# Performance work log

Hardware: AMD Instinct MI355X
Metric: run time of the kernel (lower is better)

The kernel has to match this reference:

```python
import jax, jax.numpy as jnp
import numpy as np
import math

D_MODEL = 512
NUM_HEADS = 8
HEAD_DIM = D_MODEL // NUM_HEADS
B, L = 2, 2048
LN_EPS = 1e-5
DEN_EPS = 1e-5


def setup_inputs() -> dict:
    key = jax.random.key(0)
    ks = jax.random.split(key, 6)
    s = 1.0 / math.sqrt(D_MODEL)
    return {
        "x": jax.random.normal(ks[0], (B, L, D_MODEL), dtype=jnp.float32),
        "Wqkv": jax.random.normal(ks[1], (D_MODEL, 3 * D_MODEL), dtype=jnp.float32) * s,
        "bqkv": jnp.zeros((3 * D_MODEL,), dtype=jnp.float32),
        "Wout": jax.random.normal(ks[2], (D_MODEL, D_MODEL), dtype=jnp.float32) * s,
        "bout": jnp.zeros((D_MODEL,), dtype=jnp.float32),
        "ln_gamma": jnp.ones((D_MODEL,), dtype=jnp.float32),
        "ln_beta": jnp.zeros((D_MODEL,), dtype=jnp.float32),
        "decay_logits": jnp.full((NUM_HEADS,), 5.0, dtype=jnp.float32),
    }


def reference(x, Wqkv, bqkv, Wout, bout, ln_gamma, ln_beta, decay_logits):
    Bv, Lv, D = x.shape
    H = decay_logits.shape[0]
    E = D // H

    qkv = x @ Wqkv + bqkv                                   # [B,L,3D]
    q, k, v = jnp.split(qkv, 3, axis=-1)
    q = q.reshape(Bv, Lv, H, E)
    k = k.reshape(Bv, Lv, H, E)
    v = v.reshape(Bv, Lv, H, E)

    # ELU feature map + 1 -> positive features; scale q by 1/sqrt(E)
    q = (jax.nn.elu(q) + 1.0) / jnp.sqrt(jnp.asarray(E, x.dtype))
    k = jax.nn.elu(k) + 1.0

    lambdas = jax.nn.sigmoid(decay_logits).reshape(1, 1, H, 1)   # [1,1,H,1]
    t = jnp.arange(Lv, dtype=x.dtype).reshape(1, Lv, 1, 1)       # [1,L,1,1]
    decay_k = jnp.power(lambdas, -t)   # lambda^{-t}
    decay_q = jnp.power(lambdas, t)    # lambda^{t}

    k_dec = k * decay_k                                          # [B,L,H,E]
    kv = jnp.einsum('blhe,blhf->blhef', k_dec, v)                # [B,L,H,E,E]
    memory = jnp.cumsum(kv, axis=1)                              # prefix-sum scan over L
    k_sum = jnp.cumsum(k_dec, axis=1)                            # [B,L,H,E]

    q_dec = q * decay_q
    num = jnp.einsum('blhe,blhef->blhf', q_dec, memory)          # [B,L,H,E]
    den = jnp.einsum('blhe,blhe->blh', q_dec, k_sum)[..., None] + DEN_EPS
    out = (num / den).reshape(Bv, Lv, D)

    out = out @ Wout + bout

    # LayerNorm (eval mode; dropout is identity)
    mu = jnp.mean(out, axis=-1, keepdims=True)
    var = jnp.var(out, axis=-1, keepdims=True)
    out = (out - mu) / jnp.sqrt(var + LN_EPS) * ln_gamma + ln_beta
    return out
```

## Files before the change

### kernel.cpp

```cpp
#include <hip/hip_runtime.h>
#include <math.h>

#define B_ 2
#define L_ 2048
#define D_ 512
#define H_ 8
#define E_ 64
#define CHUNK 32
#define NCH 64
#define DEN_EPS_ 1e-5f
#define LN_EPS_ 1e-5f

typedef __bf16 bf16x8 __attribute__((ext_vector_type(8)));
typedef __bf16 bf16x4 __attribute__((ext_vector_type(4)));
typedef float  f32x4  __attribute__((ext_vector_type(4)));

__device__ __forceinline__ float sigm(float x) { return 1.f / (1.f + expf(-x)); }
__device__ __forceinline__ float elu1(float x) { return x > 0.f ? x + 1.f : expf(x); }

__global__ __launch_bounds__(256) void k_transpose_both(
    const float* __restrict__ W1, __bf16* __restrict__ D1,
    const float* __restrict__ W2, __bf16* __restrict__ D2)
{
    const float* src; __bf16* dst; int N;
    if (blockIdx.z == 0) { src = W1; dst = D1; N = 1536; }
    else                 { if (blockIdx.x >= 8) return; src = W2; dst = D2; N = 512; }
    const int K = 512;

    __shared__ __bf16 tile[64][68];
    const int kb = blockIdx.y * 64, nb = blockIdx.x * 64;
    const int t = threadIdx.x;
    const int rr = t >> 4, cc4 = (t & 15) * 4;
#pragma unroll
    for (int p = 0; p < 4; p++) {
        int k = rr + p * 16;
        float4 v = *(const float4*)&src[(size_t)(kb + k) * N + nb + cc4];
        tile[k][cc4 + 0] = (__bf16)v.x;
        tile[k][cc4 + 1] = (__bf16)v.y;
        tile[k][cc4 + 2] = (__bf16)v.z;
        tile[k][cc4 + 3] = (__bf16)v.w;
    }
    __syncthreads();
#pragma unroll
    for (int p = 0; p < 4; p++) {
        int n = rr + p * 16;
        bf16x4 o;
        o[0] = tile[cc4 + 0][n];
        o[1] = tile[cc4 + 1][n];
        o[2] = tile[cc4 + 2][n];
        o[3] = tile[cc4 + 3][n];
        *(bf16x4*)&dst[(size_t)(nb + n) * K + kb + cc4] = o;
    }
}

__global__ __launch_bounds__(256) void k_mfma_qkv(
    const float* __restrict__ X, const __bf16* __restrict__ Bt,
    const float* __restrict__ bias,
    __bf16* __restrict__ Qb, __bf16* __restrict__ Kb, __bf16* __restrict__ Vb)
{
    __shared__ __bf16 Al[128 * 32];
    __shared__ __bf16 Bl[128 * 32];
    const int t = threadIdx.x;
    const int w = t >> 6, lane = t & 63;
    const int wm = w >> 1, wn = w & 1;
    const int ll = lane & 15, quad = lane >> 4;
    const int m0 = blockIdx.y * 128, n0 = blockIdx.x * 128;

    f32x4 acc[4][4] = {};
    const int sr = t >> 2, sk = (t & 3) * 8;

    for (int k0 = 0; k0 < D_; k0 += 32) {
#pragma unroll
        for (int half = 0; half < 2; half++) {
            const float* ap = X + (size_t)(m0 + sr + half * 64) * D_ + k0 + sk;
            float4 a0 = *(const float4*)ap;
            float4 a1 = *(const float4*)(ap + 4);
            bf16x8 o;
            o[0] = (__bf16)a0.x; o[1] = (__bf16)a0.y; o[2] = (__bf16)a0.z; o[3] = (__bf16)a0.w;
            o[4] = (__bf16)a1.x; o[5] = (__bf16)a1.y; o[6] = (__bf16)a1.z; o[7] = (__bf16)a1.w;
            *(bf16x8*)&Al[(sr + half * 64) * 32 + sk] = o;
        }
        *(bf16x8*)&Bl[sr * 32 + sk]        = *(const bf16x8*)&Bt[(size_t)(n0 + sr) * D_ + k0 + sk];
        *(bf16x8*)&Bl[(sr + 64) * 32 + sk] = *(const bf16x8*)&Bt[(size_t)(n0 + sr + 64) * D_ + k0 + sk];
        __syncthreads();
#pragma unroll
        for (int im = 0; im < 4; im++) {
            bf16x8 a = *(const bf16x8*)&Al[(wm * 64 + im * 16 + ll) * 32 + quad * 8];
#pragma unroll
            for (int in = 0; in < 4; in++) {
                bf16x8 b = *(const bf16x8*)&Bl[(wn * 64 + in * 16 + ll) * 32 + quad * 8];
                acc[im][in] = __builtin_amdgcn_mfma_f32_16x16x32_bf16(a, b, acc[im][in], 0, 0, 0);
            }
        }
        __syncthreads();
    }

    const int sec = n0 >> 9;
    __bf16* base = (sec == 0 ? Qb : (sec == 1 ? Kb : Vb));
#pragma unroll
    for (int im = 0; im < 4; im++) {
#pragma unroll
        for (int in = 0; in < 4; in++) {
            int n = n0 + wn * 64 + in * 16 + ll;
            int d = n & 511, h = d >> 6, e = d & 63;
            float bv = bias[n];
#pragma unroll
            for (int r = 0; r < 4; r++) {
                int m = m0 + wm * 64 + im * 16 + quad * 4 + r;
                int bb = m >> 11, l = m & 2047;
                float v = acc[im][in][r] + bv;
                if (sec == 0)      v = elu1(v) * 0.125f;
                else if (sec == 1) v = elu1(v);
                base[((size_t)((bb * H_ + h) * L_ + l)) * E_ + e] = (__bf16)v;
            }
        }
    }
}

__global__ __launch_bounds__(256) void k_chunk_g(
    const __bf16* __restrict__ Kb, const __bf16* __restrict__ Vb,
    const float* __restrict__ dl,
    __bf16* __restrict__ Gnb, float* __restrict__ gn)
{
    __shared__ __bf16 Kwt[64][40];
    __shared__ __bf16 Vt[64][40];
    const int t  = threadIdx.x;
    const int bx = blockIdx.x;
    const int n = bx & 63, h = (bx >> 6) & 7, bb = bx >> 9;
    const int bh = bb * H_ + h;
    const float lam = sigm(dl[h]);

    {
        int i = t & 31, e0 = (t >> 5) * 8;
        size_t src = ((size_t)bh * L_ + n * CHUNK + i) * E_ + e0;
        float wk = powf(lam, (float)(CHUNK - 1 - i));
        bf16x8 k8 = *(const bf16x8*)&Kb[src];
        bf16x8 v8 = *(const bf16x8*)&Vb[src];
#pragma unroll
        for (int q = 0; q < 8; q++) {
            Kwt[e0 + q][i] = (__bf16)((float)k8[q] * wk);
            Vt[e0 + q][i]  = v8[q];
        }
    }
    __syncthreads();

    const int w = t >> 6, lane = t & 63;
    const int wm = w >> 1, wn = w & 1;
    const int ll = lane & 15, quad = lane >> 4;

    bf16x8 af[2], bf_[2];
#pragma unroll
    for (int a = 0; a < 2; a++) {
        af[a]  = *(const bf16x8*)&Kwt[wm * 32 + a * 16 + ll][quad * 8];
        bf_[a] = *(const bf16x8*)&Vt[wn * 32 + a * 16 + ll][quad * 8];
    }
    f32x4 acc[2][2] = {};
#pragma unroll
    for (int a = 0; a < 2; a++)
#pragma unroll
        for (int b = 0; b < 2; b++)
            acc[a][b] = __builtin_amdgcn_mfma_f32_16x16x32_bf16(af[a], bf_[b], acc[a][b], 0, 0, 0);

    size_t gbase = ((size_t)bh * NCH + n) * 4096;
#pragma unroll
    for (int a = 0; a < 2; a++)
#pragma unroll
        for (int b = 0; b < 2; b++)
#pragma unroll
            for (int r = 0; r < 4; r++) {
                int e = wm * 32 + a * 16 + quad * 4 + r;
                int f = wn * 32 + b * 16 + ll;
                Gnb[gbase + (size_t)e * 64 + f] = (__bf16)acc[a][b][r];
            }

    if (t < 64) {
        float ga = 0.f;
#pragma unroll
        for (int k8 = 0; k8 < 4; k8++) {
            bf16x8 kk = *(const bf16x8*)&Kwt[t][k8 * 8];
#pragma unroll
            for (int q = 0; q < 8; q++) ga += (float)kk[q];
        }
        gn[((size_t)bh * NCH + n) * E_ + t] = ga;
    }
}

__global__ __launch_bounds__(64) void k_scan_par(
    const __bf16* __restrict__ Gnb, const float* __restrict__ gn,
    const float* __restrict__ dl,
    __bf16* __restrict__ Sb, float* __restrict__ zl)
{
    const int t  = threadIdx.x;
    const int bh = blockIdx.x >> 6;
    const int e  = blockIdx.x & 63;
    const float lam = sigm(dl[bh & 7]);
    const float dC  = powf(lam, (float)CHUNK);

    float s = 0.f, zs = 0.f;
    const size_t base = ((size_t)bh * NCH) * 4096 + (size_t)e * 64 + t;
    float g = (float)Gnb[base];
    for (int n = 0; n < NCH; n++) {
        size_t off = base + (size_t)n * 4096;
        float gnext = (n < NCH - 1) ? (float)Gnb[off + 4096] : 0.f;
        Sb[off] = (__bf16)(lam * s);
        s = fmaf(dC, s, g);
        g = gnext;
        if (t == 0) {
            size_t zo = ((size_t)bh * NCH + n) * E_ + e;
            zl[zo] = lam * zs;
            zs = fmaf(dC, zs, gn[zo]);
        }
    }
}

__global__ __launch_bounds__(256) void k_attn(
    const __bf16* __restrict__ Qb, const __bf16* __restrict__ Kb,
    const __bf16* __restrict__ Vb,
    const __bf16* __restrict__ Sb, const float* __restrict__ zl,
    const float* __restrict__ dl, __bf16* __restrict__ Out)
{
    __shared__ __bf16 Qw[32][64];
    __shared__ __bf16 Kw[32][64];
    __shared__ __bf16 Vt[64][40];
    __shared__ __bf16 SbT[64][72];
    __shared__ __bf16 A1[32][40];
    __shared__ float  den[32];
    __shared__ float  zz[64];

    const int t  = threadIdx.x;
    const int bx = blockIdx.x;
    const int n = bx & 63, h = (bx >> 6) & 7, bb = bx >> 9;
    const int bh = bb * H_ + h;
    const float lam = sigm(dl[h]);

    {
        int i = t >> 3, e0 = (t & 7) * 8;
        size_t src = ((size_t)bh * L_ + n * CHUNK + i) * E_ + e0;
        float wq = powf(lam, (float)i);
        float wk = powf(lam, -(float)i);
        bf16x8 q8 = *(const bf16x8*)&Qb[src];
        bf16x8 k8 = *(const bf16x8*)&Kb[src];
        bf16x8 v8 = *(const bf16x8*)&Vb[src];
        bf16x8 qo, ko;
#pragma unroll
        for (int q = 0; q < 8; q++) {
            qo[q] = (__bf16)((float)q8[q] * wq);
            ko[q] = (__bf16)((float)k8[q] * wk);
            Vt[e0 + q][i] = v8[q];
        }
        *(bf16x8*)&Qw[i][e0] = qo;
        *(bf16x8*)&Kw[i][e0] = ko;

        int e = t >> 2, f0 = (t & 3) * 16;
        size_t sbase = ((size_t)bh * NCH + n) * 4096;
        bf16x8 s0 = *(const bf16x8*)&Sb[sbase + (size_t)e * 64 + f0];
        bf16x8 s1 = *(const bf16x8*)&Sb[sbase + (size_t)e * 64 + f0 + 8];
#pragma unroll
        for (int q = 0; q < 8; q++) {
            SbT[f0 + q][e]     = s0[q];
            SbT[f0 + 8 + q][e] = s1[q];
        }
        if (t < 64) zz[t] = zl[((size_t)bh * NCH + n) * E_ + t];
    }
    __syncthreads();

    const int w = t >> 6, lane = t & 63;
    const int ll = lane & 15, quad = lane >> 4;

    {
        const int wm = w >> 1, wn = w & 1;
        f32x4 accA = {};
#pragma unroll
        for (int ks = 0; ks < 2; ks++) {
            bf16x8 a = *(const bf16x8*)&Qw[wm * 16 + ll][ks * 32 + quad * 8];
            bf16x8 b = *(const bf16x8*)&Kw[wn * 16 + ll][ks * 32 + quad * 8];
            accA = __builtin_amdgcn_mfma_f32_16x16x32_bf16(a, b, accA, 0, 0, 0);
        }
        int j = wn * 16 + ll;
#pragma unroll
        for (int r = 0; r < 4; r++) {
            int i = wm * 16 + quad * 4 + r;
            A1[i][j] = (__bf16)(j <= i ? accA[r] : 0.f);
        }
    }
    __syncthreads();

    if (t < 32) {
        float rs = 0.f;
#pragma unroll
        for (int k8 = 0; k8 < 4; k8++) {
            bf16x8 aa = *(const bf16x8*)&A1[t][k8 * 8];
#pragma unroll
            for (int q = 0; q < 8; q++) rs += (float)aa[q];
        }
        float qz = 0.f;
#pragma unroll
        for (int e8 = 0; e8 < 8; e8++) {
            bf16x8 qq = *(const bf16x8*)&Qw[t][e8 * 8];
#pragma unroll
            for (int q = 0; q < 8; q++) qz += (float)qq[q] * zz[e8 * 8 + q];
        }
        den[t] = rs + qz + DEN_EPS_;
    }

    const int fw = w * 16;
    f32x4 acc1[2] = {}, acc2[2] = {};
    {
        bf16x8 bV = *(const bf16x8*)&Vt[fw + ll][quad * 8];
#pragma unroll
        for (int im = 0; im < 2; im++) {
            bf16x8 aA = *(const bf16x8*)&A1[im * 16 + ll][quad * 8];
            acc1[im] = __builtin_amdgcn_mfma_f32_16x16x32_bf16(aA, bV, acc1[im], 0, 0, 0);
        }
#pragma unroll
        for (int ks = 0; ks < 2; ks++) {
            bf16x8 bS = *(const bf16x8*)&SbT[fw + ll][ks * 32 + quad * 8];
#pragma unroll
            for (int im = 0; im < 2; im++) {
                bf16x8 aQ = *(const bf16x8*)&Qw[im * 16 + ll][ks * 32 + quad * 8];
                acc2[im] = __builtin_amdgcn_mfma_f32_16x16x32_bf16(aQ, bS, acc2[im], 0, 0, 0);
            }
        }
    }
    __syncthreads();

#pragma unroll
    for (int im = 0; im < 2; im++)
#pragma unroll
        for (int r = 0; r < 4; r++) {
            int i = im * 16 + quad * 4 + r;
            float o = (acc1[im][r] + acc2[im][r]) / den[i];
            Out[((size_t)bb * L_ + n * CHUNK + i) * D_ + h * E_ + fw + ll] = (__bf16)o;
        }
}

__global__ __launch_bounds__(256) void k_mfma_out_ln(
    const __bf16* __restrict__ Ab, const __bf16* __restrict__ Bt,
    const float* __restrict__ bias, const float* __restrict__ gam,
    const float* __restrict__ bet, float* __restrict__ Y)
{
    __shared__ __bf16 Al[32 * 32];
    __shared__ __bf16 Bl[512 * 32];
    __shared__ float gaml[512], betl[512], bl[512];
    __shared__ float redS[4][32], redQ[4][32];
    __shared__ float mv[32][2];

    const int t = threadIdx.x;
    const int w = t >> 6, lane = t & 63;
    const int ll = lane & 15, quad = lane >> 4;
    const int m0 = blockIdx.x * 32;

    {
        float2 g = *(const float2*)&gam[t * 2];
        float2 b2 = *(const float2*)&bet[t * 2];
        float2 bo = *(const float2*)&bias[t * 2];
        gaml[t * 2] = g.x;  gaml[t * 2 + 1] = g.y;
        betl[t * 2] = b2.x; betl[t * 2 + 1] = b2.y;
        bl[t * 2]   = bo.x; bl[t * 2 + 1]   = bo.y;
    }

    f32x4 acc[2][8] = {};
    const int sr = t >> 2, sk = (t & 3) * 8;

    for (int k0 = 0; k0 < D_; k0 += 32) {
        if (t < 128)
            *(bf16x8*)&Al[sr * 32 + sk] = *(const bf16x8*)&Ab[(size_t)(m0 + sr) * D_ + k0 + sk];
#pragma unroll
        for (int p = 0; p < 8; p++)
            *(bf16x8*)&Bl[(sr + p * 64) * 32 + sk] =
                *(const bf16x8*)&Bt[(size_t)(sr + p * 64) * D_ + k0 + sk];
        __syncthreads();
#pragma unroll
        for (int im = 0; im < 2; im++) {
            bf16x8 a = *(const bf16x8*)&Al[(im * 16 + ll) * 32 + quad * 8];
#pragma unroll
            for (int in = 0; in < 8; in++) {
                bf16x8 b = *(const bf16x8*)&Bl[(w * 128 + in * 16 + ll) * 32 + quad * 8];
                acc[im][in] = __builtin_amdgcn_mfma_f32_16x16x32_bf16(a, b, acc[im][in], 0, 0, 0);
            }
        }
        __syncthreads();
    }

    float vals[2][8][4];
    float ps[2][4] = {}, pq[2][4] = {};
#pragma unroll
    for (int im = 0; im < 2; im++)
#pragma unroll
        for (int in = 0; in < 8; in++) {
            int col = w * 128 + in * 16 + ll;
            float bv = bl[col];
#pragma unroll
            for (int r = 0; r < 4; r++) {
                float v = acc[im][in][r] + bv;
                vals[im][in][r] = v;
                ps[im][r] += v;
                pq[im][r] += v * v;
            }
        }
#pragma unroll
    for (int im = 0; im < 2; im++)
#pragma unroll
        for (int r = 0; r < 4; r++) {
            float s = ps[im][r], q = pq[im][r];
            s += __shfl_xor(s, 1); q += __shfl_xor(q, 1);
            s += __shfl_xor(s, 2); q += __shfl_xor(q, 2);
            s += __shfl_xor(s, 4); q += __shfl_xor(q, 4);
            s += __shfl_xor(s, 8); q += __shfl_xor(q, 8);
            if (ll == 0) {
                int row = im * 16 + quad * 4 + r;
                redS[w][row] = s;
                redQ[w][row] = q;
            }
        }
    __syncthreads();
    if (t < 32) {
        float S = redS[0][t] + redS[1][t] + redS[2][t] + redS[3][t];
        float Q = redQ[0][t] + redQ[1][t] + redQ[2][t] + redQ[3][t];
        float mu  = S * (1.f / 512.f);
        float var = Q * (1.f / 512.f) - mu * mu;
        mv[t][0] = mu;
        mv[t][1] = rsqrtf(var + LN_EPS_);
    }
    __syncthreads();
#pragma unroll
    for (int im = 0; im < 2; im++)
#pragma unroll
        for (int r = 0; r < 4; r++) {
            int row = im * 16 + quad * 4 + r;
            float mu = mv[row][0], rs = mv[row][1];
#pragma unroll
            for (int in = 0; in < 8; in++) {
                int col = w * 128 + in * 16 + ll;
                Y[(size_t)(m0 + row) * D_ + col] =
                    (vals[im][in][r] - mu) * rs * gaml[col] + betl[col];
            }
        }
}

extern "C" void kernel_launch(void* const* d_in, const int* in_sizes, int n_in,
                              void* d_out, int out_size, void* d_ws, size_t ws_size,
                              hipStream_t stream)
{
    const float* x    = (const float*)d_in[0];
    const float* Wqkv = (const float*)d_in[1];
    const float* bqkv = (const float*)d_in[2];
    const float* Wout = (const float*)d_in[3];
    const float* bout = (const float*)d_in[4];
    const float* gam  = (const float*)d_in[5];
    const float* bet  = (const float*)d_in[6];
    const float* dl   = (const float*)d_in[7];
    float* out = (float*)d_out;

    const size_t NBHLE = (size_t)B_ * H_ * L_ * E_;
    const size_t NG    = (size_t)B_ * H_ * NCH * E_ * E_;
    const size_t Ng    = (size_t)B_ * H_ * NCH * E_;

    char* p = (char*)d_ws;
    __bf16* Gnb = (__bf16*)p;    p += NG * 2;
    __bf16* Sb  = (__bf16*)p;    p += NG * 2;
    float*  gn  = (float*)p;     p += Ng * 4;
    float*  zl  = (float*)p;     p += Ng * 4;
    __bf16* Qb  = (__bf16*)p;    p += NBHLE * 2;
    __bf16* Kb  = (__bf16*)p;    p += NBHLE * 2;
    __bf16* Vb  = (__bf16*)p;    p += NBHLE * 2;
    __bf16* WqkvT = (__bf16*)p;  p += (size_t)1536 * 512 * 2;
    __bf16* WoutT = (__bf16*)p;  p += (size_t)512 * 512 * 2;
    __bf16* Ao    = (__bf16*)p;  p += NBHLE * 2;

    dim3 blk(256);
    k_transpose_both<<<dim3(24, 8, 2), blk, 0, stream>>>(Wqkv, WqkvT, Wout, WoutT);
    k_mfma_qkv      <<<dim3(12, 32),   blk, 0, stream>>>(x, WqkvT, bqkv, Qb, Kb, Vb);
    k_chunk_g       <<<dim3(1024),     blk, 0, stream>>>(Kb, Vb, dl, Gnb, gn);
    k_scan_par      <<<dim3(1024),     dim3(64), 0, stream>>>(Gnb, gn, dl, Sb, zl);
    k_attn          <<<dim3(1024),     blk, 0, stream>>>(Qb, Kb, Vb, Sb, zl, dl, Ao);
    k_mfma_out_ln   <<<dim3(128),      blk, 0, stream>>>(Ao, WoutT, bout, gam, bet, out);
}
```

Measured before the change: 158.0 us.

## Prefetch GEMM tiles into registers, transpose chunk state layout, parallelize normalizer scan

Both MFMA GEMM kernels now load the next K-tile from global memory into registers while the current tile is being computed, so global latency overlaps with MFMA work. The chunk state matrices are stored transposed (f-major), which lets the attention kernel copy them into shared memory with vector stores instead of scattered element transposes. The state scan now loads all 64 chunk values up front into a fully unrolled register array. The normalizer scan is replaced by a 64-lane shuffle-based parallel prefix scan in place of a serial loop on one thread. This raises register pressure in the GEMMs and the scan kernel.

Result: faster. 131.4 us (-16.9%).

```diff
diff --git a/kernel.cpp b/kernel.cpp
--- a/kernel.cpp
+++ b/kernel.cpp
@@ -69,20 +69,34 @@
     f32x4 acc[4][4] = {};
     const int sr = t >> 2, sk = (t & 3) * 8;
 
+    float4 pa0[2], pa1[2];
+    bf16x8 pb[2];
+    auto fetch = [&](int k0) {
+#pragma unroll
+        for (int h2 = 0; h2 < 2; h2++) {
+            const float* ap = X + (size_t)(m0 + sr + h2 * 64) * D_ + k0 + sk;
+            pa0[h2] = *(const float4*)ap;
+            pa1[h2] = *(const float4*)(ap + 4);
+        }
+        pb[0] = *(const bf16x8*)&Bt[(size_t)(n0 + sr) * D_ + k0 + sk];
+        pb[1] = *(const bf16x8*)&Bt[(size_t)(n0 + sr + 64) * D_ + k0 + sk];
+    };
+
+    fetch(0);
     for (int k0 = 0; k0 < D_; k0 += 32) {
 #pragma unroll
-        for (int half = 0; half < 2; half++) {
-            const float* ap = X + (size_t)(m0 + sr + half * 64) * D_ + k0 + sk;
-            float4 a0 = *(const float4*)ap;
-            float4 a1 = *(const float4*)(ap + 4);
+        for (int h2 = 0; h2 < 2; h2++) {
             bf16x8 o;
-            o[0] = (__bf16)a0.x; o[1] = (__bf16)a0.y; o[2] = (__bf16)a0.z; o[3] = (__bf16)a0.w;
-            o[4] = (__bf16)a1.x; o[5] = (__bf16)a1.y; o[6] = (__bf16)a1.z; o[7] = (__bf16)a1.w;
-            *(bf16x8*)&Al[(sr + half * 64) * 32 + sk] = o;
-        }
-        *(bf16x8*)&Bl[sr * 32 + sk]        = *(const bf16x8*)&Bt[(size_t)(n0 + sr) * D_ + k0 + sk];
-        *(bf16x8*)&Bl[(sr + 64) * 32 + sk] = *(const bf16x8*)&Bt[(size_t)(n0 + sr + 64) * D_ + k0 + sk];
+            o[0] = (__bf16)pa0[h2].x; o[1] = (__bf16)pa0[h2].y;
+            o[2] = (__bf16)pa0[h2].z; o[3] = (__bf16)pa0[h2].w;
+            o[4] = (__bf16)pa1[h2].x; o[5] = (__bf16)pa1[h2].y;
+            o[6] = (__bf16)pa1[h2].z; o[7] = (__bf16)pa1[h2].w;
+            *(bf16x8*)&Al[(sr + h2 * 64) * 32 + sk] = o;
+        }
+        *(bf16x8*)&Bl[sr * 32 + sk]        = pb[0];
+        *(bf16x8*)&Bl[(sr + 64) * 32 + sk] = pb[1];
         __syncthreads();
+        if (k0 + 32 < D_) fetch(k0 + 32);
 #pragma unroll
         for (int im = 0; im < 4; im++) {
             bf16x8 a = *(const bf16x8*)&Al[(wm * 64 + im * 16 + ll) * 32 + quad * 8];
@@ -120,7 +134,7 @@
 __global__ __launch_bounds__(256) void k_chunk_g(
     const __bf16* __restrict__ Kb, const __bf16* __restrict__ Vb,
     const float* __restrict__ dl,
-    __bf16* __restrict__ Gnb, float* __restrict__ gn)
+    __bf16* __restrict__ Gt, float* __restrict__ gn)
 {
     __shared__ __bf16 Kwt[64][40];
     __shared__ __bf16 Vt[64][40];
@@ -151,8 +165,8 @@
     bf16x8 af[2], bf_[2];
 #pragma unroll
     for (int a = 0; a < 2; a++) {
-        af[a]  = *(const bf16x8*)&Kwt[wm * 32 + a * 16 + ll][quad * 8];
-        bf_[a] = *(const bf16x8*)&Vt[wn * 32 + a * 16 + ll][quad * 8];
+        af[a]  = *(const bf16x8*)&Vt[wm * 32 + a * 16 + ll][quad * 8];
+        bf_[a] = *(const bf16x8*)&Kwt[wn * 32 + a * 16 + ll][quad * 8];
     }
     f32x4 acc[2][2] = {};
 #pragma unroll
@@ -168,9 +182,9 @@
         for (int b = 0; b < 2; b++)
 #pragma unroll
             for (int r = 0; r < 4; r++) {
-                int e = wm * 32 + a * 16 + quad * 4 + r;
-                int f = wn * 32 + b * 16 + ll;
-                Gnb[gbase + (size_t)e * 64 + f] = (__bf16)acc[a][b][r];
+                int f = wm * 32 + a * 16 + quad * 4 + r;
+                int e = wn * 32 + b * 16 + ll;
+                Gt[gbase + (size_t)f * 64 + e] = (__bf16)acc[a][b][r];
             }
 
     if (t < 64) {
@@ -186,31 +200,40 @@
 }
 
 __global__ __launch_bounds__(64) void k_scan_par(
-    const __bf16* __restrict__ Gnb, const float* __restrict__ gn,
+    const __bf16* __restrict__ Gt, const float* __restrict__ gn,
     const float* __restrict__ dl,
     __bf16* __restrict__ Sb, float* __restrict__ zl)
 {
-    const int t  = threadIdx.x;
+    const int lane = threadIdx.x;
     const int bh = blockIdx.x >> 6;
-    const int e  = blockIdx.x & 63;
+    const int j  = blockIdx.x & 63;
     const float lam = sigm(dl[bh & 7]);
     const float dC  = powf(lam, (float)CHUNK);
 
-    float s = 0.f, zs = 0.f;
-    const size_t base = ((size_t)bh * NCH) * 4096 + (size_t)e * 64 + t;
-    float g = (float)Gnb[base];
+    const size_t base = ((size_t)bh * NCH) * 4096 + (size_t)j * 64 + lane;
+
+    __bf16 g[NCH];
+#pragma unroll
+    for (int n = 0; n < NCH; n++) g[n] = Gt[base + (size_t)n * 4096];
+
+    float s = 0.f;
+#pragma unroll
     for (int n = 0; n < NCH; n++) {
-        size_t off = base + (size_t)n * 4096;
-        float gnext = (n < NCH - 1) ? (float)Gnb[off + 4096] : 0.f;
-        Sb[off] = (__bf16)(lam * s);
-        s = fmaf(dC, s, g);
-        g = gnext;
-        if (t == 0) {
-            size_t zo = ((size_t)bh * NCH + n) * E_ + e;
-            zl[zo] = lam * zs;
-            zs = fmaf(dC, zs, gn[zo]);
-        }
-    }
+        Sb[base + (size_t)n * 4096] = (__bf16)(lam * s);
+        s = fmaf(dC, s, (float)g[n]);
+    }
+
+    float gv = gn[((size_t)bh * NCH + lane) * E_ + j];
+    float wf = dC;
+#pragma unroll
+    for (int k = 1; k < 64; k <<= 1) {
+        float up = __shfl_up(gv, k);
+        if (lane >= k) gv = fmaf(wf, up, gv);
+        wf = wf * wf;
+    }
+    float zex = __shfl_up(gv, 1);
+    if (lane == 0) zex = 0.f;
+    zl[((size_t)bh * NCH + lane) * E_ + j] = lam * zex;
 }
 
 __global__ __launch_bounds__(256) void k_attn(
@@ -251,15 +274,12 @@
         *(bf16x8*)&Qw[i][e0] = qo;
         *(bf16x8*)&Kw[i][e0] = ko;
 
-        int e = t >> 2, f0 = (t & 3) * 16;
+        int f = t >> 2, e00 = (t & 3) * 16;
         size_t sbase = ((size_t)bh * NCH + n) * 4096;
-        bf16x8 s0 = *(const bf16x8*)&Sb[sbase + (size_t)e * 64 + f0];
-        bf16x8 s1 = *(const bf16x8*)&Sb[sbase + (size_t)e * 64 + f0 + 8];
-#pragma unroll
-        for (int q = 0; q < 8; q++) {
-            SbT[f0 + q][e]     = s0[q];
-            SbT[f0 + 8 + q][e] = s1[q];
-        }
+        bf16x8 s0 = *(const bf16x8*)&Sb[sbase + (size_t)f * 64 + e00];
+        bf16x8 s1 = *(const bf16x8*)&Sb[sbase + (size_t)f * 64 + e00 + 8];
+        *(bf16x8*)&SbT[f][e00]     = s0;
+        *(bf16x8*)&SbT[f][e00 + 8] = s1;
         if (t < 64) zz[t] = zl[((size_t)bh * NCH + n) * E_ + t];
     }
     __syncthreads();
@@ -362,14 +382,25 @@
     f32x4 acc[2][8] = {};
     const int sr = t >> 2, sk = (t & 3) * 8;
 
+    bf16x8 pA;
+    bf16x8 pB[8];
+    auto fetch = [&](int k0) {
+        if (t < 128)
+            pA = *(const bf16x8*)&Ab[(size_t)(m0 + sr) * D_ + k0 + sk];
+#pragma unroll
+        for (int p = 0; p < 8; p++)
+            pB[p] = *(const bf16x8*)&Bt[(size_t)(sr + p * 64) * D_ + k0 + sk];
+    };
+
+    fetch(0);
     for (int k0 = 0; k0 < D_; k0 += 32) {
         if (t < 128)
-            *(bf16x8*)&Al[sr * 32 + sk] = *(const bf16x8*)&Ab[(size_t)(m0 + sr) * D_ + k0 + sk];
+            *(bf16x8*)&Al[sr * 32 + sk] = pA;
 #pragma unroll
         for (int p = 0; p < 8; p++)
-            *(bf16x8*)&Bl[(sr + p * 64) * 32 + sk] =
-                *(const bf16x8*)&Bt[(size_t)(sr + p * 64) * D_ + k0 + sk];
+            *(bf16x8*)&Bl[(sr + p * 64) * 32 + sk] = pB[p];
         __syncthreads();
+        if (k0 + 32 < D_) fetch(k0 + 32);
 #pragma unroll
         for (int im = 0; im < 2; im++) {
             bf16x8 a = *(const bf16x8*)&Al[(im * 16 + ll) * 32 + quad * 8];
@@ -457,7 +488,7 @@
     const size_t Ng    = (size_t)B_ * H_ * NCH * E_;
 
     char* p = (char*)d_ws;
-    __bf16* Gnb = (__bf16*)p;    p += NG * 2;
+    __bf16* Gt  = (__bf16*)p;    p += NG * 2;
     __bf16* Sb  = (__bf16*)p;    p += NG * 2;
     float*  gn  = (float*)p;     p += Ng * 4;
     float*  zl  = (float*)p;     p += Ng * 4;
@@ -471,8 +502,8 @@
     dim3 blk(256);
     k_transpose_both<<<dim3(24, 8, 2), blk, 0, stream>>>(Wqkv, WqkvT, Wout, WoutT);
     k_mfma_qkv      <<<dim3(12, 32),   blk, 0, stream>>>(x, WqkvT, bqkv, Qb, Kb, Vb);
-    k_chunk_g       <<<dim3(1024),     blk, 0, stream>>>(Kb, Vb, dl, Gnb, gn);
-    k_scan_par      <<<dim3(1024),     dim3(64), 0, stream>>>(Gnb, gn, dl, Sb, zl);
+    k_chunk_g       <<<dim3(1024),     blk, 0, stream>>>(Kb, Vb, dl, Gt, gn);
+    k_scan_par      <<<dim3(1024),     dim3(64), 0, stream>>>(Gt, gn, dl, Sb, zl);
     k_attn          <<<dim3(1024),     blk, 0, stream>>>(Qb, Kb, Vb, Sb, zl, dl, Ao);
     k_mfma_out_ln   <<<dim3(128),      blk, 0, stream>>>(Ao, WoutT, bout, gam, bet, out);
 }
```
